# Kernel tuning notes

Hardware: AMD Instinct MI355X
Metric: run time of the kernel (lower is better)

Reference implementation:

```python
import jax, jax.numpy as jnp
import numpy as np

ALPHA = 0.7
BETA = 0.3
GAMMA = 1.0
EPS = 1e-07


def setup_inputs() -> dict:
    key = jax.random.key(0)
    k1, k2 = jax.random.split(key)
    B, C, H, W = 8, 19, 512, 512
    inputs = jax.random.normal(k1, (B, C, H, W), dtype=jnp.float32)
    targets = jax.random.randint(k2, (B, H, W), 0, C, dtype=jnp.int64)
    return {"inputs": inputs, "targets": targets}


def reference(inputs, targets):
    # inputs: [B, C, H, W] logits; targets: [B, H, W] int labels
    B, C = inputs.shape[0], inputs.shape[1]
    probs = jax.nn.softmax(inputs, axis=1)  # [B, C, H, W]
    # one-hot target per class: [B, C, H, W]
    tgt = (targets[:, None, :, :] == jnp.arange(C)[None, :, None, None]).astype(probs.dtype)
    # per (b, c) reductions over spatial dims
    TP = jnp.sum(probs * tgt, axis=(2, 3))          # [B, C]
    FP = jnp.sum((1.0 - tgt) * probs, axis=(2, 3))  # [B, C]
    FN = jnp.sum(tgt * (1.0 - probs), axis=(2, 3))  # [B, C]
    tversky = (TP + EPS) / (TP + ALPHA * FN + BETA * FP + EPS)
    focal_tversky = (1.0 - tversky) ** GAMMA
    return jnp.sum(focal_tversky) / B
```

## Files before the change

kernel.cpp:

```cpp
#include <hip/hip_runtime.h>

#define NCLS 19
#define HWPIX (512 * 512)
#define NB 8
#define ALPHA_C 0.7f
#define BETA_C 0.3f
#define EPS_C 1e-7f
#define L2E 1.44269504088896f

typedef float v2f __attribute__((ext_vector_type(2)));

__global__ __launch_bounds__(256, 3) void ftl_reduce(
    const float* __restrict__ x,
    const int* __restrict__ tgt,
    float* __restrict__ part,
    int PB) {
  const int b = blockIdx.x / PB;
  const int blk = blockIdx.x % PB;
  const int tid = threadIdx.x;

  __shared__ float sTPb[NCLS][32];
  __shared__ int sNb[NCLS][32];
  __shared__ float sS[NCLS];
  for (int i = tid; i < NCLS * 32; i += 256) {
    (&sTPb[0][0])[i] = 0.f;
    (&sNb[0][0])[i] = 0;
  }
  if (tid < NCLS) sS[tid] = 0.f;
  __syncthreads();

  const int quadsPerBlock = (HWPIX / 4) / PB;
  const int qbase = blk * quadsPerBlock;
  const float* xb = x + (size_t)b * NCLS * HWPIX;
  const int* tb = tgt + (size_t)b * HWPIX;
  const int cp = tid & 31;

  v2f S2[NCLS];
#pragma unroll
  for (int c = 0; c < NCLS; ++c) S2[c] = (v2f){0.f, 0.f};

  for (int q = tid; q < quadsPerBlock; q += 256) {
    const int pix = (qbase + q) * 4;
    const int4 t = *reinterpret_cast<const int4*>(tb + pix);

    v2f ea[NCLS], eb[NCLS];
    v2f sea = (v2f){0.f, 0.f}, seb = (v2f){0.f, 0.f};
#pragma unroll
    for (int c = 0; c < NCLS; ++c) {
      const float4 xv = *reinterpret_cast<const float4*>(xb + (size_t)c * HWPIX + pix);
      const v2f a = (v2f){xv.x, xv.y} * L2E;
      const v2f bb = (v2f){xv.z, xv.w} * L2E;
      ea[c] = (v2f){__builtin_amdgcn_exp2f(a.x), __builtin_amdgcn_exp2f(a.y)};
      eb[c] = (v2f){__builtin_amdgcn_exp2f(bb.x), __builtin_amdgcn_exp2f(bb.y)};
      sea += ea[c];
      seb += eb[c];
    }
    const v2f inva = (v2f){__builtin_amdgcn_rcpf(sea.x), __builtin_amdgcn_rcpf(sea.y)};
    const v2f invb = (v2f){__builtin_amdgcn_rcpf(seb.x), __builtin_amdgcn_rcpf(seb.y)};
#pragma unroll
    for (int c = 0; c < NCLS; ++c) {
      S2[c] += ea[c] * inva;
      S2[c] += eb[c] * invb;
    }

    const v2f xta = (v2f){xb[(size_t)t.x * HWPIX + pix + 0],
                          xb[(size_t)t.y * HWPIX + pix + 1]} * L2E;
    const v2f xtb = (v2f){xb[(size_t)t.z * HWPIX + pix + 2],
                          xb[(size_t)t.w * HWPIX + pix + 3]} * L2E;
    const v2f pta = (v2f){__builtin_amdgcn_exp2f(xta.x),
                          __builtin_amdgcn_exp2f(xta.y)} * inva;
    const v2f ptb = (v2f){__builtin_amdgcn_exp2f(xtb.x),
                          __builtin_amdgcn_exp2f(xtb.y)} * invb;
    atomicAdd(&sTPb[t.x][cp], pta.x);
    atomicAdd(&sTPb[t.y][cp], pta.y);
    atomicAdd(&sTPb[t.z][cp], ptb.x);
    atomicAdd(&sTPb[t.w][cp], ptb.y);
    atomicAdd(&sNb[t.x][cp], 1);
    atomicAdd(&sNb[t.y][cp], 1);
    atomicAdd(&sNb[t.z][cp], 1);
    atomicAdd(&sNb[t.w][cp], 1);
  }

#pragma unroll
  for (int c = 0; c < NCLS; ++c) {
    float Sc = S2[c].x + S2[c].y;
    for (int off = 32; off; off >>= 1) Sc += __shfl_down(Sc, off);
    if ((tid & 63) == 0) atomicAdd(&sS[c], Sc);
  }
  __syncthreads();
  if (tid < NCLS) {
    float tp = 0.f;
    int n = 0;
#pragma unroll
    for (int i = 0; i < 32; ++i) { tp += sTPb[tid][i]; n += sNb[tid][i]; }
    float* p = part + (size_t)blockIdx.x * (3 * NCLS);
    p[tid] = sS[tid];
    p[NCLS + tid] = tp;
    p[2 * NCLS + tid] = (float)n;
  }
}

__global__ __launch_bounds__(640) void ftl_final(
    const float* __restrict__ part, float* __restrict__ out, int PB) {
  const int tid = threadIdx.x;
  const int pair = tid >> 2;
  const int s = tid & 3;
  float v = 0.f;
  if (pair < NB * NCLS) {
    const int b = pair / NCLS;
    const int c = pair % NCLS;
    float S = 0.f, TP = 0.f, Nc = 0.f;
    for (int p = s; p < PB; p += 4) {
      const float* q = part + (size_t)(b * PB + p) * (3 * NCLS);
      S += q[c];
      TP += q[NCLS + c];
      Nc += q[2 * NCLS + c];
    }
    S += __shfl_xor(S, 1);  S += __shfl_xor(S, 2);
    TP += __shfl_xor(TP, 1); TP += __shfl_xor(TP, 2);
    Nc += __shfl_xor(Nc, 1); Nc += __shfl_xor(Nc, 2);
    if (s == 0) {
      const float FPv = S - TP;
      const float FNv = Nc - TP;
      const float tv = (TP + EPS_C) / (TP + ALPHA_C * FNv + BETA_C * FPv + EPS_C);
      v = 1.0f - tv;
    }
  }
  for (int off = 32; off; off >>= 1) v += __shfl_down(v, off);
  __shared__ float wsum[10];
  if ((tid & 63) == 0) wsum[tid >> 6] = v;
  __syncthreads();
  if (tid == 0) {
    float r = 0.f;
#pragma unroll
    for (int w = 0; w < 10; ++w) r += wsum[w];
    out[0] = r / (float)NB;
  }
}

extern "C" void kernel_launch(void* const* d_in, const int* in_sizes, int n_in,
                              void* d_out, int out_size, void* d_ws, size_t ws_size,
                              hipStream_t stream) {
  const float* x = (const float*)d_in[0];
  const int* tgt = (const int*)d_in[1];
  float* out = (float*)d_out;
  float* part = (float*)d_ws;

  int PB = 128;
  while (PB > 1 && (size_t)(NB * PB * 3 * NCLS * sizeof(float)) > ws_size) PB >>= 1;

  ftl_reduce<<<NB * PB, 256, 0, stream>>>(x, tgt, part, PB);
  ftl_final<<<1, 640, 0, stream>>>(part, out, PB);
}
```

Measured before the change: 56.36 us.

## Fuse final reduction into main kernel via last-block atomic counter

Removes the separate finalize kernel. Each block now bumps a global atomic counter, and the last block to finish reduces all partials and writes the loss. The number of blocks per batch is also fixed at 64 instead of up to 128. This halves the grid, and a memset is added to reset the counter on every call. The intent is to save one kernel launch, at the cost of less parallelism in the main pass and a serial final reduction done by one block.

After: 49.41 us. 12.3% less time.

```diff
diff --git a/kernel.cpp b/kernel.cpp
--- a/kernel.cpp
+++ b/kernel.cpp
@@ -3,6 +3,7 @@
 #define NCLS 19
 #define HWPIX (512 * 512)
 #define NB 8
+#define PB 64
 #define ALPHA_C 0.7f
 #define BETA_C 0.3f
 #define EPS_C 1e-7f
@@ -10,11 +11,12 @@
 
 typedef float v2f __attribute__((ext_vector_type(2)));
 
-__global__ __launch_bounds__(256, 3) void ftl_reduce(
+__global__ __launch_bounds__(256, 3) void ftl_fused(
     const float* __restrict__ x,
     const int* __restrict__ tgt,
     float* __restrict__ part,
-    int PB) {
+    int* __restrict__ counter,
+    float* __restrict__ out) {
   const int b = blockIdx.x / PB;
   const int blk = blockIdx.x % PB;
   const int tid = threadIdx.x;
@@ -98,44 +100,39 @@
     p[NCLS + tid] = tp;
     p[2 * NCLS + tid] = (float)n;
   }
-}
 
-__global__ __launch_bounds__(640) void ftl_final(
-    const float* __restrict__ part, float* __restrict__ out, int PB) {
-  const int tid = threadIdx.x;
-  const int pair = tid >> 2;
-  const int s = tid & 3;
+  __syncthreads();
+  __shared__ int lastFlag;
+  if (tid == 0) {
+    __threadfence();
+    lastFlag = (atomicAdd(counter, 1) == (NB * PB - 1));
+  }
+  __syncthreads();
+  if (!lastFlag) return;
+  __threadfence();
+
   float v = 0.f;
-  if (pair < NB * NCLS) {
-    const int b = pair / NCLS;
-    const int c = pair % NCLS;
+  if (tid < NB * NCLS) {
+    const int bb = tid / NCLS;
+    const int c = tid % NCLS;
     float S = 0.f, TP = 0.f, Nc = 0.f;
-    for (int p = s; p < PB; p += 4) {
-      const float* q = part + (size_t)(b * PB + p) * (3 * NCLS);
+#pragma unroll 16
+    for (int p = 0; p < PB; ++p) {
+      const float* q = part + (size_t)(bb * PB + p) * (3 * NCLS);
       S += q[c];
       TP += q[NCLS + c];
       Nc += q[2 * NCLS + c];
     }
-    S += __shfl_xor(S, 1);  S += __shfl_xor(S, 2);
-    TP += __shfl_xor(TP, 1); TP += __shfl_xor(TP, 2);
-    Nc += __shfl_xor(Nc, 1); Nc += __shfl_xor(Nc, 2);
-    if (s == 0) {
-      const float FPv = S - TP;
-      const float FNv = Nc - TP;
-      const float tv = (TP + EPS_C) / (TP + ALPHA_C * FNv + BETA_C * FPv + EPS_C);
-      v = 1.0f - tv;
-    }
+    const float FPv = S - TP;
+    const float FNv = Nc - TP;
+    const float tv = (TP + EPS_C) / (TP + ALPHA_C * FNv + BETA_C * FPv + EPS_C);
+    v = 1.0f - tv;
   }
   for (int off = 32; off; off >>= 1) v += __shfl_down(v, off);
-  __shared__ float wsum[10];
+  __shared__ float wsum[4];
   if ((tid & 63) == 0) wsum[tid >> 6] = v;
   __syncthreads();
-  if (tid == 0) {
-    float r = 0.f;
-#pragma unroll
-    for (int w = 0; w < 10; ++w) r += wsum[w];
-    out[0] = r / (float)NB;
-  }
+  if (tid == 0) out[0] = (wsum[0] + wsum[1] + wsum[2] + wsum[3]) / (float)NB;
 }
 
 extern "C" void kernel_launch(void* const* d_in, const int* in_sizes, int n_in,
@@ -145,10 +142,8 @@
   const int* tgt = (const int*)d_in[1];
   float* out = (float*)d_out;
   float* part = (float*)d_ws;
+  int* counter = (int*)(part + NB * PB * 3 * NCLS);
 
-  int PB = 128;
-  while (PB > 1 && (size_t)(NB * PB * 3 * NCLS * sizeof(float)) > ws_size) PB >>= 1;
-
-  ftl_reduce<<<NB * PB, 256, 0, stream>>>(x, tgt, part, PB);
-  ftl_final<<<1, 640, 0, stream>>>(part, out, PB);
+  hipMemsetAsync(counter, 0, sizeof(int), stream);
+  ftl_fused<<<NB * PB, 256, 0, stream>>>(x, tgt, part, counter, out);
 }
```
